# Optimization experiments

Measured on AMD Instinct MI355X. Metric: run time of the kernel, lower is better.

## Reference

```python
import jax, jax.numpy as jnp
import numpy as np

NEG_INF = jnp.float32(-9e15)

def gat_layer(x, adj_mask, W, a, alpha):
    # x: [N, F_in]; W: [H, F_in, F_out]; a: [H, 2*F_out]; adj_mask: [N, N] bool
    H, _, O = W.shape
    h = jnp.einsum('nf,hfo->hno', x, W)            # [H, N, O]
    a_src, a_dst = a[:, :O], a[:, O:]              # [H, O] each
    e_src = jnp.einsum('hno,ho->hn', h, a_src)     # [H, N]
    e_dst = jnp.einsum('hno,ho->hn', h, a_dst)     # [H, N]
    e = jax.nn.leaky_relu(e_src[:, :, None] + e_dst[:, None, :], negative_slope=alpha)
    e = jnp.where(adj_mask[None, :, :], e, NEG_INF)  # mask non-edges
    attn = jax.nn.softmax(e, axis=-1)              # [H, N, N]
    out = jnp.einsum('hnm,hmo->hno', attn, h)      # [H, N, O]
    return out.mean(axis=0)                        # average heads -> [N, O]

def setup_inputs() -> dict:
    key = jax.random.key(0)
    ks = jax.random.split(key, 6)
    N, F_IN, F_HID, F_CLS, H = 4096, 512, 256, 16, 4
    x = jax.random.normal(ks[0], (N, F_IN), dtype=jnp.float32)
    adj = jax.random.randint(ks[1], (N, N), 0, 2, dtype=jnp.int32)
    W1 = jax.random.normal(ks[2], (H, F_IN, F_HID), dtype=jnp.float32) * 0.05
    a1 = jax.random.normal(ks[3], (H, 2 * F_HID), dtype=jnp.float32) * 0.05
    W2 = jax.random.normal(ks[4], (1, F_HID, F_CLS), dtype=jnp.float32) * 0.05
    a2 = jax.random.normal(ks[5], (1, 2 * F_CLS), dtype=jnp.float32) * 0.05
    return {"x": x, "adj": adj, "W1": W1, "a1": a1, "W2": W2, "a2": a2}

def reference(x, adj, W1, a1, W2, a2):
    alpha = 0.2
    adj_mask = adj > 0
    h = jax.nn.relu(gat_layer(x, adj_mask, W1, a1, alpha))        # layer1 + ReLU
    out = gat_layer(h, adj_mask, W2, a2, alpha)                    # layer2
    return jax.nn.log_softmax(out, axis=1)                         # [N, nclass]
```

## Files before the change

kernel.cpp:

```cpp
#include <hip/hip_runtime.h>
#include <stdint.h>

#define N_NODES 4096
#define F_IN    512
#define F_HID   256
#define F_CLS   16
#define NHEAD   4
#define ALPHA   0.2f
#define LOG2E   1.4426950408889634f

typedef __attribute__((ext_vector_type(8))) short short8;
typedef __attribute__((ext_vector_type(4))) float f32x4;

__device__ __forceinline__ float bf2f(unsigned short h) {
    unsigned u = ((unsigned)h) << 16; float f; __builtin_memcpy(&f, &u, 4); return f;
}
__device__ __forceinline__ unsigned short f2bf(float f) {
    unsigned u; __builtin_memcpy(&u, &f, 4);
    u += 0x7fffu + ((u >> 16) & 1u);
    return (unsigned short)(u >> 16);
}
__device__ __forceinline__ float lo_bf(unsigned u) { u <<= 16;          float f; __builtin_memcpy(&f,&u,4); return f; }
__device__ __forceinline__ float hi_bf(unsigned u) { u &= 0xffff0000u;  float f; __builtin_memcpy(&f,&u,4); return f; }

__device__ __forceinline__ void async_cp16(void* lds, const void* g) {
    __builtin_amdgcn_global_load_lds(
        (const __attribute__((address_space(1))) unsigned int*)g,
        (__attribute__((address_space(3))) unsigned int*)lds,
        16, 0, 0);
}

#define PREP_BM_BLOCKS   16384
#define PREP_CV_BLOCKS   1296
#define PREP_Z_BLOCKS    4
__global__ __launch_bounds__(256) void k_prep(const int* __restrict__ adj,
                                              const float* __restrict__ x,
                                              const float* __restrict__ W1,
                                              const float* __restrict__ W2,
                                              unsigned long long* __restrict__ bm,
                                              unsigned short* __restrict__ xb,
                                              unsigned short* __restrict__ W1t,
                                              float* __restrict__ W2t,
                                              float* __restrict__ ez) {
    int b = blockIdx.x;
    if (b < PREP_BM_BLOCKS) {
        int wv = threadIdx.x >> 6, lane = threadIdx.x & 63;
        int idx0 = b * 1024 + wv * 256;
        const int* p = adj + idx0 + lane;
        unsigned long long m0 = __ballot(p[0]   > 0);
        unsigned long long m1 = __ballot(p[64]  > 0);
        unsigned long long m2 = __ballot(p[128] > 0);
        unsigned long long m3 = __ballot(p[192] > 0);
        if (lane == 0) {
            int w = idx0 >> 6;
            bm[w] = m0; bm[w+1] = m1; bm[w+2] = m2; bm[w+3] = m3;
        }
        return;
    }
    if (b < PREP_BM_BLOCKS + PREP_CV_BLOCKS) {
        int tid = (b - PREP_BM_BLOCKS) * 256 + threadIdx.x;
        const int NXV = (N_NODES * F_IN) / 8;
        const int NW1 = NHEAD * 64 * F_HID;
        if (tid < NXV) {
            float4 a = *(const float4*)&x[tid * 8];
            float4 c = *(const float4*)&x[tid * 8 + 4];
            uint4 w;
            w.x = (unsigned)f2bf(a.x) | ((unsigned)f2bf(a.y) << 16);
            w.y = (unsigned)f2bf(a.z) | ((unsigned)f2bf(a.w) << 16);
            w.z = (unsigned)f2bf(c.x) | ((unsigned)f2bf(c.y) << 16);
            w.w = (unsigned)f2bf(c.z) | ((unsigned)f2bf(c.w) << 16);
            *(uint4*)&xb[tid * 8] = w;
        } else if (tid < NXV + NW1) {
            int j = tid - NXV;
            int o = j & 255, f8 = (j >> 8) & 63, h = j >> 14;
            float v[8];
            #pragma unroll
            for (int k = 0; k < 8; ++k)
                v[k] = W1[(size_t)(h * F_IN + f8 * 8 + k) * F_HID + o];
            uint4 w;
            w.x = (unsigned)f2bf(v[0]) | ((unsigned)f2bf(v[1]) << 16);
            w.y = (unsigned)f2bf(v[2]) | ((unsigned)f2bf(v[3]) << 16);
            w.z = (unsigned)f2bf(v[4]) | ((unsigned)f2bf(v[5]) << 16);
            w.w = (unsigned)f2bf(v[6]) | ((unsigned)f2bf(v[7]) << 16);
            *(uint4*)&W1t[(size_t)(h * F_HID + o) * F_IN + f8 * 8] = w;
        } else {
            int j = tid - NXV - NW1;
            if (j < F_HID * F_CLS) {
                int o = j >> 4, c = j & 15;
                W2t[c * F_HID + o] = W2[j];
            }
        }
        return;
    }
    {
        int zb = b - PREP_BM_BLOCKS - PREP_CV_BLOCKS;
        float4* z4 = (float4*)ez;
        #pragma unroll
        for (int r = 0; r < 8; ++r)
            z4[zb * 2048 + r * 256 + threadIdx.x] = make_float4(0.f, 0.f, 0.f, 0.f);
    }
}

__global__ __launch_bounds__(256, 4) void k_gemm1(const unsigned short* __restrict__ xb,
                                                  const unsigned short* __restrict__ W1t,
                                                  const float* __restrict__ a1,
                                                  unsigned short* __restrict__ h1t,
                                                  float* __restrict__ es1,
                                                  float* __restrict__ ed1) {
    __shared__ unsigned short Sld[2][6144];
    const int t = threadIdx.x;
    const int lane = t & 63, wv = t >> 6, quad = lane >> 4, l15 = lane & 15;
    const int wn = wv & 1, wo = wv >> 1;
    const int n0 = blockIdx.x * 128;
    const int oo0 = blockIdx.y * 64;
    const int h = blockIdx.z;
    const int kl = (lane >> 4) * 8;

    const unsigned short* gs[3];
    int loff[3];
    #pragma unroll
    for (int s = 0; s < 3; ++s) {
        int c = wv * 3 + s;
        loff[s] = c * 512;
        gs[s] = (c < 8)
            ? (xb  + (size_t)(n0 + c * 16 + l15) * F_IN + kl)
            : (W1t + (size_t)(h * F_HID + oo0 + (c - 8) * 16 + l15) * F_IN + kl);
    }
    #pragma unroll
    for (int s = 0; s < 3; ++s) async_cp16(&Sld[0][loff[s]], gs[s]);

    f32x4 acc[4][2] = {};
    for (int it = 0; it < 16; ++it) {
        const int cur = it & 1;
        __syncthreads();
        if (it + 1 < 16) {
            const int off = (it + 1) * 32;
            #pragma unroll
            for (int s = 0; s < 3; ++s) async_cp16(&Sld[1 - cur][loff[s]], gs[s] + off);
        }
        short8 bfw[2];
        #pragma unroll
        for (int mi = 0; mi < 2; ++mi)
            bfw[mi] = *(const short8*)&Sld[cur][(8 + wo * 2 + mi) * 512 + lane * 8];
        #pragma unroll
        for (int ni = 0; ni < 4; ++ni) {
            short8 af = *(const short8*)&Sld[cur][(wn * 4 + ni) * 512 + lane * 8];
            #pragma unroll
            for (int mi = 0; mi < 2; ++mi)
                acc[ni][mi] = __builtin_amdgcn_mfma_f32_16x16x32_bf16(af, bfw[mi], acc[ni][mi], 0, 0, 0);
        }
    }
    #pragma unroll
    for (int ni = 0; ni < 4; ++ni)
      #pragma unroll
      for (int mi = 0; mi < 2; ++mi) {
        int o = oo0 + wo * 32 + mi * 16 + l15;
        int nb = n0 + wn * 64 + ni * 16 + quad * 4;
        uint2 uu;
        uu.x = (unsigned)f2bf(acc[ni][mi][0]) | ((unsigned)f2bf(acc[ni][mi][1]) << 16);
        uu.y = (unsigned)f2bf(acc[ni][mi][2]) | ((unsigned)f2bf(acc[ni][mi][3]) << 16);
        *(uint2*)&h1t[(size_t)(h * F_HID + o) * N_NODES + nb] = uu;
      }
    float a1s[2], a1d[2];
    #pragma unroll
    for (int mi = 0; mi < 2; ++mi) {
        int o = oo0 + wo * 32 + mi * 16 + l15;
        a1s[mi] = a1[h * 2 * F_HID + o] * LOG2E;
        a1d[mi] = a1[h * 2 * F_HID + F_HID + o] * LOG2E;
    }
    #pragma unroll
    for (int ni = 0; ni < 4; ++ni) {
        #pragma unroll
        for (int rg = 0; rg < 4; ++rg) {
            float es = acc[ni][0][rg] * a1s[0] + acc[ni][1][rg] * a1s[1];
            float ed = acc[ni][0][rg] * a1d[0] + acc[ni][1][rg] * a1d[1];
            #pragma unroll
            for (int off = 1; off < 16; off <<= 1) {
                es += __shfl_xor(es, off, 64);
                ed += __shfl_xor(ed, off, 64);
            }
            if (l15 == 0) {
                int n = n0 + wn * 64 + ni * 16 + quad * 4 + rg;
                atomicAdd(&es1[h * N_NODES + n], es);
                atomicAdd(&ed1[h * N_NODES + n], ed);
            }
        }
    }
}

__global__ __launch_bounds__(512, 2) void k_attn1(const unsigned short* __restrict__ h1t,
                                                  const float* __restrict__ es1,
                                                  const float* __restrict__ ed1,
                                                  const unsigned char* __restrict__ bmb,
                                                  unsigned short* __restrict__ C1p,
                                                  float* __restrict__ l1p) {
    __shared__ unsigned short Bld[2][8192];
    const int t = threadIdx.x;
    const int lane = t & 63, wv = t >> 6, quad = lane >> 4, l15 = lane & 15;
    const int m0 = blockIdx.x * 256;
    const int h = blockIdx.y;
    const int kz = blockIdx.z;
    const int mb0 = kz * 1024;

    const int m_r0 = m0 + wv * 32 + l15;
    const int m_r1 = m_r0 + 16;
    const float esr0 = es1[h * N_NODES + m_r0];
    const float esr1 = es1[h * N_NODES + m_r1];
    const unsigned char* bp0 = bmb + (size_t)m_r0 * (N_NODES / 8);
    const unsigned char* bp1 = bmb + (size_t)m_r1 * (N_NODES / 8);
    const float* edb = ed1 + h * N_NODES;

    const unsigned short* gb0 = h1t + (size_t)(h * F_HID + wv * 16 + l15) * N_NODES + (lane >> 4) * 8;
    const unsigned short* gb1 = h1t + (size_t)(h * F_HID + (wv + 8) * 16 + l15) * N_NODES + (lane >> 4) * 8;
    async_cp16(&Bld[0][wv * 512], gb0 + mb0);
    async_cp16(&Bld[0][(wv + 8) * 512], gb1 + mb0);

    f32x4 acc[16][2] = {};
    float lsum0 = 0.f, lsum1 = 0.f;
    for (int it = 0; it < 32; ++it) {
        const int cur = it & 1;
        const int mb = mb0 + it * 32;
        __syncthreads();
        if (it + 1 < 32) {
            async_cp16(&Bld[1 - cur][wv * 512], gb0 + mb + 32);
            async_cp16(&Bld[1 - cur][(wv + 8) * 512], gb1 + mb + 32);
        }
        float4 e0 = *(const float4*)&edb[mb + quad * 8];
        float4 e1v = *(const float4*)&edb[mb + quad * 8 + 4];
        float ev[8] = {e0.x, e0.y, e0.z, e0.w, e1v.x, e1v.y, e1v.z, e1v.w};
        unsigned bb0 = bp0[(mb >> 3) + quad];
        unsigned bb1 = bp1[(mb >> 3) + quad];
        unsigned up0[8], up1[8];
        #pragma unroll
        for (int j = 0; j < 8; ++j) {
            float s0 = esr0 + ev[j]; s0 = fmaxf(s0, ALPHA * s0);
            float p0 = ((bb0 >> j) & 1u) ? __builtin_amdgcn_exp2f(s0) : 0.f;
            unsigned u0; __builtin_memcpy(&u0, &p0, 4); u0 &= 0xffff0000u;
            float pt0; __builtin_memcpy(&pt0, &u0, 4);
            lsum0 += pt0; up0[j] = u0;
            float s1 = esr1 + ev[j]; s1 = fmaxf(s1, ALPHA * s1);
            float p1 = ((bb1 >> j) & 1u) ? __builtin_amdgcn_exp2f(s1) : 0.f;
            unsigned u1; __builtin_memcpy(&u1, &p1, 4); u1 &= 0xffff0000u;
            float pt1; __builtin_memcpy(&pt1, &u1, 4);
            lsum1 += pt1; up1[j] = u1;
        }
        int pk0[4], pk1[4];
        #pragma unroll
        for (int j = 0; j < 4; ++j) {
            pk0[j] = __builtin_amdgcn_perm(up0[2*j+1], up0[2*j], 0x07060302u);
            pk1[j] = __builtin_amdgcn_perm(up1[2*j+1], up1[2*j], 0x07060302u);
        }
        short8 bfrag0, bfrag1;
        __builtin_memcpy(&bfrag0, pk0, 16);
        __builtin_memcpy(&bfrag1, pk1, 16);
        #pragma unroll
        for (int ot = 0; ot < 16; ++ot) {
            short8 af = *(const short8*)&Bld[cur][ot * 512 + lane * 8];
            acc[ot][0] = __builtin_amdgcn_mfma_f32_16x16x32_bf16(af, bfrag0, acc[ot][0], 0, 0, 0);
            acc[ot][1] = __builtin_amdgcn_mfma_f32_16x16x32_bf16(af, bfrag1, acc[ot][1], 0, 0, 0);
        }
    }
    lsum0 += __shfl_xor(lsum0, 16, 64); lsum0 += __shfl_xor(lsum0, 32, 64);
    lsum1 += __shfl_xor(lsum1, 16, 64); lsum1 += __shfl_xor(lsum1, 32, 64);
    if (quad == 0) {
        l1p[(size_t)(kz * NHEAD + h) * N_NODES + m_r0] = lsum0;
        l1p[(size_t)(kz * NHEAD + h) * N_NODES + m_r1] = lsum1;
    }
    unsigned short* Cb = C1p + (size_t)(kz * NHEAD + h) * N_NODES * F_HID;
    #pragma unroll
    for (int ot = 0; ot < 16; ++ot)
      #pragma unroll
      for (int mi = 0; mi < 2; ++mi) {
        int m = (mi == 0) ? m_r0 : m_r1;
        int o0 = ot * 16 + quad * 4;
        uint2 uu;
        uu.x = (unsigned)f2bf(acc[ot][mi][0]) | ((unsigned)f2bf(acc[ot][mi][1]) << 16);
        uu.y = (unsigned)f2bf(acc[ot][mi][2]) | ((unsigned)f2bf(acc[ot][mi][3]) << 16);
        *(uint2*)&Cb[(size_t)m * F_HID + o0] = uu;
      }
}

__global__ __launch_bounds__(256) void k_reduce1(const unsigned short* __restrict__ C1p,
                                                 const float* __restrict__ l1p,
                                                 unsigned short* __restrict__ h2) {
    int t = threadIdx.x;
    int og = t & 31, nl = t >> 5;
    int n = blockIdx.x * 8 + nl;
    float acc8[8] = {};
    #pragma unroll
    for (int h = 0; h < NHEAD; ++h) {
        float den = 0.f, num[8] = {};
        #pragma unroll
        for (int kz = 0; kz < 4; ++kz) {
            den += l1p[(size_t)(kz * NHEAD + h) * N_NODES + n];
            uint4 u = *(const uint4*)&C1p[((size_t)(kz * NHEAD + h) * N_NODES + n) * F_HID + og * 8];
            num[0] += lo_bf(u.x); num[1] += hi_bf(u.x);
            num[2] += lo_bf(u.y); num[3] += hi_bf(u.y);
            num[4] += lo_bf(u.z); num[5] += hi_bf(u.z);
            num[6] += lo_bf(u.w); num[7] += hi_bf(u.w);
        }
        float rinv = 1.f / fmaxf(den, 1e-30f);
        #pragma unroll
        for (int j = 0; j < 8; ++j) acc8[j] += num[j] * rinv;
    }
    uint4 w;
    unsigned short bq[8];
    #pragma unroll
    for (int j = 0; j < 8; ++j) bq[j] = f2bf(fmaxf(acc8[j] * 0.25f, 0.f));
    w.x = (unsigned)bq[0] | ((unsigned)bq[1] << 16);
    w.y = (unsigned)bq[2] | ((unsigned)bq[3] << 16);
    w.z = (unsigned)bq[4] | ((unsigned)bq[5] << 16);
    w.w = (unsigned)bq[6] | ((unsigned)bq[7] << 16);
    *(uint4*)&h2[(size_t)n * F_HID + og * 8] = w;
}

__global__ __launch_bounds__(256) void k_h2w(const unsigned short* __restrict__ h2,
                                             const float* __restrict__ W2t,
                                             const float* __restrict__ a2,
                                             unsigned short* __restrict__ h2wt,
                                             float* __restrict__ es2, float* __restrict__ ed2) {
    int t = threadIdx.x;
    int c = t & 15, nl = t >> 4;
    int n = blockIdx.x * 16 + nl;
    const unsigned short* hrow = h2 + (size_t)n * F_HID;
    const float* wrow = W2t + c * F_HID;
    float dot = 0.f;
    for (int o = 0; o < F_HID; o += 8) {
        uint4 hu = *(const uint4*)&hrow[o];
        float4 w0 = *(const float4*)&wrow[o];
        float4 w1 = *(const float4*)&wrow[o + 4];
        dot += lo_bf(hu.x)*w0.x + hi_bf(hu.x)*w0.y + lo_bf(hu.y)*w0.z + hi_bf(hu.y)*w0.w;
        dot += lo_bf(hu.z)*w1.x + hi_bf(hu.z)*w1.y + lo_bf(hu.w)*w1.z + hi_bf(hu.w)*w1.w;
    }
    h2wt[(size_t)c * N_NODES + n] = f2bf(dot);
    float es = dot * a2[c] * LOG2E;
    float ed = dot * a2[F_CLS + c] * LOG2E;
    #pragma unroll
    for (int off = 1; off < 16; off <<= 1) {
        es += __shfl_xor(es, off, 64);
        ed += __shfl_xor(ed, off, 64);
    }
    if (c == 0) { es2[n] = es; ed2[n] = ed; }
}

__global__ __launch_bounds__(256, 4) void k_attn2(const unsigned short* __restrict__ h2wt,
                                                  const float* __restrict__ es2,
                                                  const float* __restrict__ ed2,
                                                  const unsigned char* __restrict__ bmb,
                                                  float* __restrict__ out2p,
                                                  float* __restrict__ l2p) {
    const int t = threadIdx.x;
    const int lane = t & 63, wv = t >> 6, quad = lane >> 4, l15 = lane & 15;
    const int m0 = blockIdx.x * 64;
    const int ks = blockIdx.y;
    const int m_r = m0 + wv * 16 + l15;
    const float esr = es2[m_r];
    const unsigned char* bp = bmb + (size_t)m_r * (N_NODES / 8);

    f32x4 acc = {};
    float lsum = 0.f;
    for (int it = 0; it < 16; ++it) {
        const int mb = ks * 512 + it * 32;
        float4 e0 = *(const float4*)&ed2[mb + quad * 8];
        float4 e1v = *(const float4*)&ed2[mb + quad * 8 + 4];
        float ev[8] = {e0.x, e0.y, e0.z, e0.w, e1v.x, e1v.y, e1v.z, e1v.w};
        unsigned bb = bp[(mb >> 3) + quad];
        short8 afrag;
        #pragma unroll
        for (int j = 0; j < 8; ++j) {
            float s = esr + ev[j]; s = fmaxf(s, ALPHA * s);
            float p = ((bb >> j) & 1u) ? __builtin_amdgcn_exp2f(s) : 0.f;
            lsum += p; afrag[j] = (short)f2bf(p);
        }
        short8 bfr = *(const short8*)&h2wt[(size_t)l15 * N_NODES + mb + quad * 8];
        acc = __builtin_amdgcn_mfma_f32_16x16x32_bf16(afrag, bfr, acc, 0, 0, 0);
    }
    lsum += __shfl_xor(lsum, 16, 64); lsum += __shfl_xor(lsum, 32, 64);
    if (quad == 0) l2p[(size_t)ks * N_NODES + m_r] = lsum;
    #pragma unroll
    for (int rg = 0; rg < 4; ++rg) {
        int row = m0 + wv * 16 + quad * 4 + rg;
        out2p[((size_t)ks * N_NODES + row) * F_CLS + l15] = acc[rg];
    }
}

__global__ __launch_bounds__(256) void k_final(const float* __restrict__ out2p,
                                               const float* __restrict__ l2p,
                                               float* __restrict__ out) {
    int t = threadIdx.x;
    int c = t & 15, nl = t >> 4;
    int n = blockIdx.x * 16 + nl;
    float v = 0.f, l = 0.f;
    #pragma unroll
    for (int ks = 0; ks < 8; ++ks) {
        v += out2p[((size_t)ks * N_NODES + n) * F_CLS + c];
        l += l2p[(size_t)ks * N_NODES + n];
    }
    v /= fmaxf(l, 1e-30f);
    float mx = v;
    #pragma unroll
    for (int off = 1; off < 16; off <<= 1) mx = fmaxf(mx, __shfl_xor(mx, off, 64));
    float e = __expf(v - mx);
    float se = e;
    #pragma unroll
    for (int off = 1; off < 16; off <<= 1) se += __shfl_xor(se, off, 64);
    out[(size_t)n * F_CLS + c] = v - mx - __logf(se);
}

#define OFF_BM    0ull
#define OFF_XB    2097152ull
#define OFF_W1T   6291456ull
#define OFF_W2T   7340032ull
#define OFF_ES1   7356416ull
#define OFF_ED1   7421952ull
#define OFF_ES2   7487488ull
#define OFF_ED2   7503872ull
#define OFF_L1P   7520256ull
#define OFF_L2P   7782400ull
#define OFF_H2    7910400ull
#define OFF_OUT2P 7910400ull
#define OFF_H2WT  10007552ull
#define OFF_H1T   10138624ull
#define OFF_C1P   18527232ull

extern "C" void kernel_launch(void* const* d_in, const int* in_sizes, int n_in,
                              void* d_out, int out_size, void* d_ws, size_t ws_size,
                              hipStream_t stream) {
    const float* x   = (const float*)d_in[0];
    const int*   adj = (const int*)d_in[1];
    const float* W1  = (const float*)d_in[2];
    const float* a1  = (const float*)d_in[3];
    const float* W2  = (const float*)d_in[4];
    const float* a2  = (const float*)d_in[5];
    float* out = (float*)d_out;
    char* ws = (char*)d_ws;

    unsigned long long* bm  = (unsigned long long*)(ws + OFF_BM);
    unsigned char*      bmb = (unsigned char*)(ws + OFF_BM);
    unsigned short* xb   = (unsigned short*)(ws + OFF_XB);
    unsigned short* W1t  = (unsigned short*)(ws + OFF_W1T);
    float* W2t   = (float*)(ws + OFF_W2T);
    float* es1   = (float*)(ws + OFF_ES1);
    float* ed1   = (float*)(ws + OFF_ED1);
    float* es2   = (float*)(ws + OFF_ES2);
    float* ed2   = (float*)(ws + OFF_ED2);
    float* l1p   = (float*)(ws + OFF_L1P);
    float* l2p   = (float*)(ws + OFF_L2P);
    unsigned short* h2   = (unsigned short*)(ws + OFF_H2);
    float* out2p = (float*)(ws + OFF_OUT2P);
    unsigned short* h2wt = (unsigned short*)(ws + OFF_H2WT);
    unsigned short* h1t  = (unsigned short*)(ws + OFF_H1T);
    unsigned short* C1p  = (unsigned short*)(ws + OFF_C1P);

    k_prep    <<<dim3(PREP_BM_BLOCKS + PREP_CV_BLOCKS + PREP_Z_BLOCKS), 256, 0, stream>>>(
                  adj, x, W1, W2, bm, xb, W1t, W2t, es1);
    k_gemm1   <<<dim3(32, 4, 4), 256, 0, stream>>>(xb, W1t, a1, h1t, es1, ed1);
    k_attn1   <<<dim3(16, 4, 4), 512, 0, stream>>>(h1t, es1, ed1, bmb, C1p, l1p);
    k_reduce1 <<<dim3(512),      256, 0, stream>>>(C1p, l1p, h2);
    k_h2w     <<<dim3(256),      256, 0, stream>>>(h2, W2t, a2, h2wt, es2, ed2);
    k_attn2   <<<dim3(64, 8),    256, 0, stream>>>(h2wt, es2, ed2, bmb, out2p, l2p);
    k_final   <<<dim3(256),      256, 0, stream>>>(out2p, l2p, out);
}
```

Before: 232.4 us.

## Triple-buffer LDS async loads with partial vmcnt waits in gemm1 and attn1

Both k_gemm1 and k_attn1 move from double to triple-buffered LDS staging and prefetch two tiles ahead. The blanket __syncthreads is replaced by an explicit s_waitcnt that waits only until the older async loads have landed (vmcnt 3 or 2), followed by s_barrier. The aim is to keep global-to-LDS loads in flight across iterations and hide memory latency behind MFMA work. In exchange it uses more LDS, which may reduce occupancy, and it issues wrapped-around redundant loads in the last iterations. The hand-encoded waitcnt values must also match the number of outstanding vector memory ops, including the edb and bitmask loads in attn1.

```diff
diff --git a/kernel.cpp b/kernel.cpp
--- a/kernel.cpp
+++ b/kernel.cpp
@@ -28,6 +28,19 @@
         (const __attribute__((address_space(1))) unsigned int*)g,
         (__attribute__((address_space(3))) unsigned int*)lds,
         16, 0, 0);
+}
+
+__device__ __forceinline__ void pipe_barrier_vm2() {
+    __builtin_amdgcn_sched_barrier(0);
+    __builtin_amdgcn_s_waitcnt(0x0072);
+    __builtin_amdgcn_s_barrier();
+    __builtin_amdgcn_sched_barrier(0);
+}
+__device__ __forceinline__ void pipe_barrier_vm3() {
+    __builtin_amdgcn_sched_barrier(0);
+    __builtin_amdgcn_s_waitcnt(0x0073);
+    __builtin_amdgcn_s_barrier();
+    __builtin_amdgcn_sched_barrier(0);
 }
 
 #define PREP_BM_BLOCKS   16384
@@ -107,7 +120,7 @@
                                                   unsigned short* __restrict__ h1t,
                                                   float* __restrict__ es1,
                                                   float* __restrict__ ed1) {
-    __shared__ unsigned short Sld[2][6144];
+    __shared__ unsigned short Sld[3][6144];
     const int t = threadIdx.x;
     const int lane = t & 63, wv = t >> 6, quad = lane >> 4, l15 = lane & 15;
     const int wn = wv & 1, wo = wv >> 1;
@@ -128,15 +141,18 @@
     }
     #pragma unroll
     for (int s = 0; s < 3; ++s) async_cp16(&Sld[0][loff[s]], gs[s]);
+    #pragma unroll
+    for (int s = 0; s < 3; ++s) async_cp16(&Sld[1][loff[s]], gs[s] + 32);
 
     f32x4 acc[4][2] = {};
+    int cur = 0;
     for (int it = 0; it < 16; ++it) {
-        const int cur = it & 1;
-        __syncthreads();
-        if (it + 1 < 16) {
-            const int off = (it + 1) * 32;
+        pipe_barrier_vm3();
+        {
+            const int nxt = (cur >= 1) ? cur - 1 : 2;
+            const int off = ((it + 2) & 15) * 32;
             #pragma unroll
-            for (int s = 0; s < 3; ++s) async_cp16(&Sld[1 - cur][loff[s]], gs[s] + off);
+            for (int s = 0; s < 3; ++s) async_cp16(&Sld[nxt][loff[s]], gs[s] + off);
         }
         short8 bfw[2];
         #pragma unroll
@@ -149,6 +165,7 @@
             for (int mi = 0; mi < 2; ++mi)
                 acc[ni][mi] = __builtin_amdgcn_mfma_f32_16x16x32_bf16(af, bfw[mi], acc[ni][mi], 0, 0, 0);
         }
+        cur = (cur == 2) ? 0 : cur + 1;
     }
     #pragma unroll
     for (int ni = 0; ni < 4; ++ni)
@@ -194,7 +211,7 @@
                                                   const unsigned char* __restrict__ bmb,
                                                   unsigned short* __restrict__ C1p,
                                                   float* __restrict__ l1p) {
-    __shared__ unsigned short Bld[2][8192];
+    __shared__ unsigned short Bld[3][8192];
     const int t = threadIdx.x;
     const int lane = t & 63, wv = t >> 6, quad = lane >> 4, l15 = lane & 15;
     const int m0 = blockIdx.x * 256;
@@ -214,16 +231,20 @@
     const unsigned short* gb1 = h1t + (size_t)(h * F_HID + (wv + 8) * 16 + l15) * N_NODES + (lane >> 4) * 8;
     async_cp16(&Bld[0][wv * 512], gb0 + mb0);
     async_cp16(&Bld[0][(wv + 8) * 512], gb1 + mb0);
+    async_cp16(&Bld[1][wv * 512], gb0 + mb0 + 32);
+    async_cp16(&Bld[1][(wv + 8) * 512], gb1 + mb0 + 32);
 
     f32x4 acc[16][2] = {};
     float lsum0 = 0.f, lsum1 = 0.f;
+    int cur = 0;
     for (int it = 0; it < 32; ++it) {
-        const int cur = it & 1;
         const int mb = mb0 + it * 32;
-        __syncthreads();
-        if (it + 1 < 32) {
-            async_cp16(&Bld[1 - cur][wv * 512], gb0 + mb + 32);
-            async_cp16(&Bld[1 - cur][(wv + 8) * 512], gb1 + mb + 32);
+        pipe_barrier_vm2();
+        {
+            const int nxt = (cur >= 1) ? cur - 1 : 2;
+            const int mbp = mb0 + ((it + 2) & 31) * 32;
+            async_cp16(&Bld[nxt][wv * 512], gb0 + mbp);
+            async_cp16(&Bld[nxt][(wv + 8) * 512], gb1 + mbp);
         }
         float4 e0 = *(const float4*)&edb[mb + quad * 8];
         float4 e1v = *(const float4*)&edb[mb + quad * 8 + 4];
@@ -259,6 +280,7 @@
             acc[ot][0] = __builtin_amdgcn_mfma_f32_16x16x32_bf16(af, bfrag0, acc[ot][0], 0, 0, 0);
             acc[ot][1] = __builtin_amdgcn_mfma_f32_16x16x32_bf16(af, bfrag1, acc[ot][1], 0, 0, 0);
         }
+        cur = (cur == 2) ? 0 : cur + 1;
     }
     lsum0 += __shfl_xor(lsum0, 16, 64); lsum0 += __shfl_xor(lsum0, 32, 64);
     lsum1 += __shfl_xor(lsum1, 16, 64); lsum1 += __shfl_xor(lsum1, 32, 64);
```

New measurement: 231.6 us. No clear change (-0.3%).
